# Kernel tuning notes

Hardware: AMD Instinct MI355X
Metric: run time of the kernel (lower is better)

The kernel has to match this reference:

```python
import jax, jax.numpy as jnp
import numpy as np

B, N = 4, 500
C_DIM = 256            # content_dim == feat_channels
G = 4                  # n_groups
P_IN, P_OUT = 32, 128
EFF = C_DIM // G       # 64 = eff_in_dim = eff_out_dim
TOTAL = EFF * EFF + P_IN * P_OUT   # 8192 params per group per query
STRIDES = (8, 16, 32, 64)
LVL_SHAPES = ((100, 160), (50, 80), (25, 40), (13, 20))
TAU = 2.0
LVL_MAP = 3.0          # log2(STRIDES[0]): z -> fpn level index
EPS = 1e-5


def setup_inputs() -> dict:
    key = jax.random.key(0)
    ks = jax.random.split(key, 16)
    feats = [jax.random.normal(ks[i], (B, C_DIM, h, w), jnp.float32)
             for i, (h, w) in enumerate(LVL_SHAPES)]
    query_feat = jax.random.normal(ks[4], (B, N, C_DIM), jnp.float32)
    xy = jax.random.uniform(ks[5], (B, N, 2), jnp.float32, 50.0, 1000.0)
    z = jax.random.uniform(ks[6], (B, N, 1), jnp.float32, 3.0, 6.0)
    r = jax.random.uniform(ks[7], (B, N, 1), jnp.float32, -1.0, 1.0)
    query_xyzr = jnp.concatenate([xy, z, r], -1)
    w_off = jax.random.normal(ks[8], (C_DIM, P_IN * G * 3), jnp.float32) * 0.01
    b_off = jax.random.normal(ks[9], (P_IN * G * 3,), jnp.float32) * 0.1
    w_pg = jax.random.normal(ks[10], (C_DIM, G * TOTAL), jnp.float32) * 0.02
    b_pg = jax.random.normal(ks[11], (G * TOTAL,), jnp.float32) * 0.02
    w_out = jax.random.normal(ks[12], (G * P_OUT * EFF, C_DIM), jnp.float32) * 0.005
    b_out = jnp.zeros((C_DIM,), jnp.float32)
    ln_g = jnp.ones((C_DIM,), jnp.float32)
    ln_b = jnp.zeros((C_DIM,), jnp.float32)
    return dict(feat0=feats[0], feat1=feats[1], feat2=feats[2], feat3=feats[3],
                query_feat=query_feat, query_xyzr=query_xyzr,
                w_off=w_off, b_off=b_off, w_pg=w_pg, b_pg=b_pg,
                w_out=w_out, b_out=b_out, ln_g=ln_g, ln_b=ln_b)


def _ln2d(x):
    # F.layer_norm over last TWO dims, no affine
    mu = x.mean((-2, -1), keepdims=True)
    var = jnp.mean((x - mu) ** 2, (-2, -1), keepdims=True)
    return (x - mu) * jax.lax.rsqrt(var + EPS)


def _bilinear(feat, px, py):
    # torch grid_sample(bilinear, zeros padding, align_corners=False)
    # feat: [BG, H, W, Cg]; px, py: [BG, Q] pixel coords
    BGn, H, W, Cg = feat.shape
    fflat = feat.reshape(BGn, H * W, Cg)
    bidx = jnp.arange(BGn)[:, None]
    x0 = jnp.floor(px)
    y0 = jnp.floor(py)
    wx, wy = px - x0, py - y0
    x0i, y0i = x0.astype(jnp.int32), y0.astype(jnp.int32)

    def corner(xi, yi, w):
        valid = (xi >= 0) & (xi < W) & (yi >= 0) & (yi < H)
        idx = jnp.clip(yi, 0, H - 1) * W + jnp.clip(xi, 0, W - 1)
        return fflat[bidx, idx] * (w * valid)[..., None]

    return (corner(x0i, y0i, (1 - wx) * (1 - wy)) + corner(x0i + 1, y0i, wx * (1 - wy))
            + corner(x0i, y0i + 1, (1 - wx) * wy) + corner(x0i + 1, y0i + 1, wx * wy))


def _forward(feat0, feat1, feat2, feat3, query_feat, query_xyzr,
             w_off, b_off, w_pg, b_pg, w_out, b_out, ln_g, ln_b):
    feats = (feat0, feat1, feat2, feat3)
    # --- make_sample_points ---
    off = (query_feat @ w_off + b_off).reshape(B, N, G * P_IN, 3)
    cc = query_xyzr[..., :2]
    z = query_xyzr[..., 2:3]
    r = query_xyzr[..., 3:4]
    roi_wh = (2.0 ** z) * jnp.concatenate([2.0 ** (-0.5 * r), 2.0 ** (0.5 * r)], -1)  # [B,N,2]
    sample_xy = cc[:, :, None, :] + off[..., :2] * roi_wh[:, :, None, :]   # [B,N,G*P,2]
    sample_lvl = z[:, :, None, 0:1] + off[..., 2:3]                        # [B,N,G*P,1]

    # --- sampling_3d: softmax level weights ---
    lvl = sample_lvl[..., 0] - LVL_MAP                                     # [B,N,G*P]
    grid = jnp.arange(len(STRIDES), dtype=lvl.dtype)
    lw = jax.nn.softmax(-((lvl[..., None] - grid) ** 2) / TAU, axis=-1)    # [B,N,G*P,L]

    # regroup to per-group layout [B*G, N*P, ...]
    sx = sample_xy.reshape(B, N, G, P_IN, 2).transpose(0, 2, 1, 3, 4).reshape(B * G, N * P_IN, 2)
    lw_g = lw.reshape(B, N, G, P_IN, -1).transpose(0, 2, 1, 3, 4).reshape(B * G, N * P_IN, -1)

    sampled = jnp.zeros((B * G, N * P_IN, EFF), jnp.float32)
    for li, (feat, stride) in enumerate(zip(feats, STRIDES)):
        H, W = feat.shape[2], feat.shape[3]
        fg = feat.reshape(B * G, EFF, H, W).transpose(0, 2, 3, 1)  # [BG,H,W,EFF]
        nx = sx[..., 0] / (W * stride) * 2.0 - 1.0
        ny = sx[..., 1] / (H * stride) * 2.0 - 1.0
        px = (nx + 1.0) * 0.5 * W - 0.5
        py = (ny + 1.0) * 0.5 * H - 0.5
        sampled = sampled + _bilinear(fg, px, py) * lw_g[..., li][..., None]
    # [B,N,G,P,EFF]
    x = sampled.reshape(B, G, N, P_IN, EFF).transpose(0, 2, 1, 3, 4)

    # --- AdaptiveMixing ---
    params = (query_feat @ w_pg + b_pg).reshape(B * N, G, TOTAL)
    M = params[..., :EFF * EFF].reshape(B * N, G, EFF, EFF)
    S = params[..., EFF * EFF:].reshape(B * N, G, P_OUT, P_IN)
    out = x.reshape(B * N, G, P_IN, EFF)
    out = jax.nn.relu(_ln2d(jnp.einsum('bgpc,bgcd->bgpd', out, M)))  # channel mix
    out = jax.nn.relu(_ln2d(jnp.einsum('bgop,bgpd->bgod', S, out)))  # spatial mix
    out = out.reshape(B, N, G * P_OUT * EFF) @ w_out + b_out
    q = query_feat + out

    # --- final LayerNorm(content_dim) with affine ---
    mu = q.mean(-1, keepdims=True)
    var = jnp.mean((q - mu) ** 2, -1, keepdims=True)
    return (q - mu) * jax.lax.rsqrt(var + EPS) * ln_g + ln_b


def reference(feat0, feat1, feat2, feat3, query_feat, query_xyzr,
              w_off, b_off, w_pg, b_pg, w_out, b_out, ln_g, ln_b):
    return _forward(feat0, feat1, feat2, feat3, query_feat, query_xyzr,
                    w_off, b_off, w_pg, b_pg, w_out, b_out, ln_g, ln_b)
```

## Files before the change

kernel.cpp:

```cpp
#include <hip/hip_runtime.h>
#include <hip/hip_bf16.h>
#include <cstdint>
#include <cstddef>

#define DI __device__ __forceinline__

#define NN 500
#define NQ 2000
#define GTOT 32768
#define LN_EPS 1e-5f

typedef __attribute__((ext_vector_type(8))) short short8v;
typedef __attribute__((ext_vector_type(4))) float f32x4;
typedef __attribute__((ext_vector_type(2))) float f32x2;
typedef const __attribute__((address_space(1))) void* gp1_t;
typedef __attribute__((address_space(3))) void* lp3_t;

DI unsigned short f2bf(float f){
  unsigned u = __float_as_uint(f);
  return (unsigned short)((u + 0x7fffu + ((u>>16)&1u)) >> 16);
}
DI float bf2f(unsigned short s){ return __uint_as_float(((unsigned)s)<<16); }

DI ushort4 cvt4(float4 a){
  ushort4 r; r.x=f2bf(a.x); r.y=f2bf(a.y); r.z=f2bf(a.z); r.w=f2bf(a.w); return r;
}

DI void bred256(float& s, float& s2, float* red, int tid){
  #pragma unroll
  for(int off=32; off; off>>=1){
    s  += __shfl_xor(s,  off, 64);
    s2 += __shfl_xor(s2, off, 64);
  }
  int w = tid>>6;
  if((tid&63)==0){ red[w*2]=s; red[w*2+1]=s2; }
  __syncthreads();
  s  = red[0]+red[2]+red[4]+red[6];
  s2 = red[1]+red[3]+red[5]+red[7];
  __syncthreads();
}

__global__ __launch_bounds__(384) void k_off(const float* __restrict__ qf,
    const float* __restrict__ xyzr, const float* __restrict__ w_off,
    const float* __restrict__ b_off, float2* __restrict__ xyb, float4* __restrict__ lwb){
  __shared__ float qs[8][256];
  __shared__ float os[8][384];
  int q0 = blockIdx.x*8, tid = threadIdx.x;
  for(int idx=tid; idx<2048; idx+=384){
    int qq = idx>>8, k = idx&255;
    qs[qq][k] = qf[(size_t)(q0+qq)*256 + k];
  }
  __syncthreads();
  {
    int j = tid;
    float acc[8];
    #pragma unroll
    for(int i=0;i<8;i++) acc[i]=0.f;
    for(int k=0;k<256;k++){
      float w = w_off[(size_t)k*384 + j];
      #pragma unroll
      for(int qq=0;qq<8;qq++) acc[qq] += qs[qq][k]*w;
    }
    float bb = b_off[j];
    #pragma unroll
    for(int qq=0;qq<8;qq++) os[qq][j] = acc[qq] + bb;
  }
  __syncthreads();
  for(int idx=tid; idx<1024; idx+=384){
    int qq = idx>>7, gp = idx&127;
    int q = q0+qq;
    float4 xr = *(const float4*)&xyzr[(size_t)q*4];
    float rw = exp2f(xr.z - 0.5f*xr.w);
    float rh = exp2f(xr.z + 0.5f*xr.w);
    float sx = xr.x + os[qq][gp*3+0]*rw;
    float sy = xr.y + os[qq][gp*3+1]*rh;
    float lvl = xr.z + os[qq][gp*3+2] - 3.0f;
    float d0=lvl, d1=lvl-1.f, d2=lvl-2.f, d3=lvl-3.f;
    float e0=-0.5f*d0*d0, e1=-0.5f*d1*d1, e2=-0.5f*d2*d2, e3=-0.5f*d3*d3;
    float m = fmaxf(fmaxf(e0,e1),fmaxf(e2,e3));
    float x0=expf(e0-m), x1=expf(e1-m), x2=expf(e2-m), x3=expf(e3-m);
    float inv = 1.f/(x0+x1+x2+x3);
    xyb[(size_t)q*128+gp] = make_float2(sx,sy);
    lwb[(size_t)q*128+gp] = make_float4(x0*inv, x1*inv, x2*inv, x3*inv);
  }
}

__global__ __launch_bounds__(256) void k_prep2(
    const float* __restrict__ f0, const float* __restrict__ f1,
    const float* __restrict__ f2, const float* __restrict__ f3,
    const float* __restrict__ qf, const float* __restrict__ w_pg,
    const float* __restrict__ w_out, unsigned short* __restrict__ featT,
    unsigned short* __restrict__ qfb, unsigned short* __restrict__ wpgT,
    unsigned short* __restrict__ woutT){
  __shared__ unsigned short tile[64*68];
  int bid = blockIdx.x, tid = threadIdx.x;

  if(bid < 4096){
    const float* src; unsigned short* dst; int R, C, lb;
    if(bid < 2048){ src=w_pg;  dst=wpgT;  R=256;  C=GTOT; lb=bid; }
    else          { src=w_out; dst=woutT; R=GTOT; C=256;  lb=bid-2048; }
    int ctiles = C >> 6;
    int rt = lb / ctiles, ct = lb % ctiles;
    int r0 = rt<<6, c0 = ct<<6;
    #pragma unroll
    for(int i=0;i<4;i++){
      int idx = tid + i*256;
      int r = idx >> 4, c4 = (idx & 15)*4;
      float4 v = *(const float4*)(src + (size_t)(r0+r)*C + c0 + c4);
      *(ushort4*)(tile + r*68 + c4) = cvt4(v);
    }
    __syncthreads();
    #pragma unroll
    for(int i=0;i<4;i++){
      int idx = tid + i*256;
      int cc = idx >> 4, r4 = (idx & 15)*4;
      ushort4 v;
      v.x = tile[(r4+0)*68 + cc];
      v.y = tile[(r4+1)*68 + cc];
      v.z = tile[(r4+2)*68 + cc];
      v.w = tile[(r4+3)*68 + cc];
      *(ushort4*)(dst + (size_t)(c0+cc)*R + r0 + r4) = v;
    }
  } else if(bid < 9440){
    const float* src; unsigned short* dst; int HW, nb, lb;
    int fb = bid - 4096;
    if(fb < 4000){ src=f0; dst=featT;            HW=16000; nb=250; lb=fb; }
    else if(fb < 5008){ src=f1; dst=featT+16384000; HW=4000; nb=63; lb=fb-4000; }
    else if(fb < 5264){ src=f2; dst=featT+20480000; HW=1000; nb=16; lb=fb-5008; }
    else { src=f3; dst=featT+21504000; HW=260; nb=5; lb=fb-5264; }
    int bg = lb / nb, hb = lb % nb;
    int b = bg >> 2, g = bg & 3;
    const float* s = src + ((size_t)(b*256 + g*64))*HW + hb*64;
    unsigned short* d = dst + (size_t)bg*HW*64 + (size_t)hb*64*64;
    int rem = HW - hb*64;
    #pragma unroll
    for(int i=0;i<4;i++){
      int idx = tid + i*256;
      int c = idx >> 4, h4 = (idx & 15)*4;
      if(h4 < rem){
        float4 v = *(const float4*)(s + (size_t)c*HW + h4);
        *(ushort4*)(tile + c*68 + h4) = cvt4(v);
      }
    }
    __syncthreads();
    #pragma unroll
    for(int i=0;i<4;i++){
      int idx = tid + i*256;
      int hw = idx >> 4, c4 = (idx & 15)*4;
      if(hw < rem){
        ushort4 v;
        v.x = tile[(c4+0)*68 + hw];
        v.y = tile[(c4+1)*68 + hw];
        v.z = tile[(c4+2)*68 + hw];
        v.w = tile[(c4+3)*68 + hw];
        *(ushort4*)(d + (size_t)hw*64 + c4) = v;
      }
    }
  } else {
    int idx = (bid-9440)*256 + tid;
    size_t base = (size_t)idx*8;
    int row = idx >> 5;
    ushort4 lo, hi;
    if(row < NQ){
      float4 a = *(const float4*)(qf + base);
      float4 b = *(const float4*)(qf + base + 4);
      lo = cvt4(a); hi = cvt4(b);
    } else {
      lo.x=lo.y=lo.z=lo.w=0; hi.x=hi.y=hi.z=hi.w=0;
    }
    *(ushort4*)(qfb + base) = lo;
    *(ushort4*)(qfb + base + 4) = hi;
  }
}

DI f32x4 mfma16(short8v a, short8v b, f32x4 c){
  return __builtin_amdgcn_mfma_f32_16x16x32_bf16(a, b, c, 0, 0, 0);
}

DI int swz32(int c, int r){ return c ^ (r&3) ^ ((r>>2)&3); }

DI void stageG32(const unsigned short* __restrict__ g, size_t row0, size_t ldk,
                 size_t k0, unsigned short* lds, int tid){
  int wv = tid>>6;
  #pragma unroll
  for(int i=0;i<2;i++){
    int e = i*256 + tid;
    int r = e>>2, c = e&3;
    int cs = swz32(c, r);
    const unsigned short* gp = g + (row0 + (size_t)r)*ldk + k0 + (size_t)cs*8;
    unsigned short* lp = lds + (size_t)(i*256 + wv*64)*8;
    __builtin_amdgcn_global_load_lds((gp1_t)(const void*)gp, (lp3_t)(void*)lp, 16, 0, 0);
  }
}

DI short8v frag32(const unsigned short* lds, int row, int q4){
  return *(const short8v*)(lds + (size_t)row*32 + (size_t)swz32(q4, row)*8);
}

DI void mma32(const unsigned short* lsA, const unsigned short* lsB,
              int wm, int wn, int lane, f32x4 acc[4][4]){
  int r15 = lane&15, q4 = lane>>4;
  short8v a[4], b[4];
  #pragma unroll
  for(int i=0;i<4;i++){
    a[i] = frag32(lsA, wm*64 + i*16 + r15, q4);
    b[i] = frag32(lsB, wn*64 + i*16 + r15, q4);
  }
  #pragma unroll
  for(int mi=0;mi<4;mi++)
    #pragma unroll
    for(int ni=0;ni<4;ni++)
      acc[mi][ni] = mfma16(a[mi], b[ni], acc[mi][ni]);
}

DI int xcd_remap(int bid, int nwg){
  return ((bid & 7) * (nwg >> 3)) + (bid >> 3);
}

__global__ __launch_bounds__(256, 4) void k_pgemm_mfma(const unsigned short* __restrict__ qfb,
    const unsigned short* __restrict__ wpgT, const float* __restrict__ b_pg,
    unsigned short* __restrict__ par, int qbase, int qlim, int mtiles){
  __shared__ unsigned short pool[16384];
  int bid = xcd_remap(blockIdx.x, gridDim.x);
  int mt = bid % mtiles, nt = bid / mtiles;
  size_t m0 = (size_t)mt*128, n0 = (size_t)nt*128;
  int tid = threadIdx.x, lane = tid&63, wv = tid>>6;
  int wm = wv>>1, wn = wv&1;
  int r15 = lane&15, q4 = lane>>4;
  f32x4 acc[4][4] = {};
  stageG32(qfb,  qbase+m0, 256, 0, pool, tid);
  stageG32(wpgT, n0,       256, 0, pool + 8192, tid);
  __syncthreads();
  #pragma unroll
  for(int t=0; t<8; t++){
    int co = (t&1)*4096;
    if(t<7){
      int no = ((t&1)^1)*4096;
      stageG32(qfb,  qbase+m0, 256, (size_t)(t+1)*32, pool + no, tid);
      stageG32(wpgT, n0,       256, (size_t)(t+1)*32, pool + 8192 + no, tid);
    }
    mma32(pool + co, pool + 8192 + co, wm, wn, lane, acc);
    __syncthreads();
  }
  unsigned short* es = pool;
  #pragma unroll
  for(int h=0; h<2; ++h){
    if(h) __syncthreads();
    if(wn == h){
      #pragma unroll
      for(int ni=0; ni<4; ni++){
        float bias = b_pg[(int)n0 + wn*64 + ni*16 + r15];
        #pragma unroll
        for(int mi=0; mi<4; mi++)
          #pragma unroll
          for(int j=0; j<4; j++){
            int row = wm*64 + mi*16 + q4*4 + j;
            es[row*72 + ni*16 + r15] = f2bf(acc[mi][ni][j] + bias);
          }
      }
    }
    __syncthreads();
    #pragma unroll
    for(int i=0;i<4;i++){
      int e = i*256 + tid;
      int row = e>>3, c8 = (e&7)*8;
      int rl = (int)m0 + row;
      if(qbase + rl < qlim){
        uint4 v = *(const uint4*)(es + row*72 + c8);
        *(uint4*)&par[(size_t)rl*GTOT + n0 + h*64 + c8] = v;
      }
    }
  }
}

__global__ __launch_bounds__(256, 4) void k_fgemm_mfma(const unsigned short* __restrict__ Ag,
    const unsigned short* __restrict__ woutT, float* __restrict__ part,
    int qbase, int qlim, int mtiles, int kspl){
  __shared__ unsigned short pool[16384];
  int bid = xcd_remap(blockIdx.x, gridDim.x);
  int nt = bid & 1;
  int r2 = bid >> 1;
  int mt = r2 % mtiles, ks = r2 / mtiles;
  size_t m0 = (size_t)mt*128, n0 = (size_t)nt*128;
  int tid = threadIdx.x, lane = tid&63, wv = tid>>6;
  int wm = wv>>1, wn = wv&1;
  f32x4 acc[4][4] = {};
  int klen = GTOT / kspl;
  size_t kbase = (size_t)ks*klen;
  int NT = klen >> 5;
  stageG32(Ag,    m0, GTOT, kbase, pool, tid);
  stageG32(woutT, n0, GTOT, kbase, pool + 8192, tid);
  __syncthreads();
  for(int t=0; t<NT; t++){
    int co = (t&1)*4096;
    if(t+1<NT){
      int no = ((t&1)^1)*4096;
      stageG32(Ag,    m0, GTOT, kbase + (size_t)(t+1)*32, pool + no, tid);
      stageG32(woutT, n0, GTOT, kbase + (size_t)(t+1)*32, pool + 8192 + no, tid);
    }
    mma32(pool + co, pool + 8192 + co, wm, wn, lane, acc);
    __syncthreads();
  }
  float* pp = part + (size_t)ks*NQ*256;
  int r15 = lane&15, q4 = lane>>4;
  #pragma unroll
  for(int mi=0; mi<4; mi++){
    #pragma unroll
    for(int j=0; j<4; j++){
      int rl = (int)m0 + wm*64 + mi*16 + q4*4 + j;
      int q = qbase + rl;
      if(q < qlim){
        #pragma unroll
        for(int ni=0; ni<4; ni++){
          int col = (int)n0 + wn*64 + ni*16 + r15;
          pp[(size_t)q*256 + col] = acc[mi][ni][j];
        }
      }
    }
  }
}

__global__ __launch_bounds__(256) void k_mix(const unsigned short* __restrict__ featT,
    const float2* __restrict__ xyb, const float4* __restrict__ lwb,
    const unsigned short* __restrict__ par, unsigned short* __restrict__ out2,
    int qbase){
  __shared__ __align__(16) char pool[31744];
  __shared__ float red[8];
  float* offW = (float*)pool;
  unsigned short* xs  = (unsigned short*)(pool + 4096);
  unsigned short* Ms  = (unsigned short*)(pool + 8704);
  unsigned short* o1t = (unsigned short*)(pool + 17408);
  unsigned short* Ss  = (unsigned short*)(pool + 22528);
  unsigned short* o2s = (unsigned short*)pool;

  int lq = blockIdx.x >> 2, g = blockIdx.x & 3;
  int q = qbase + lq;
  int b = q / NN;
  int bg = b*4 + g;
  int tid = threadIdx.x;
  int lane = tid & 63, wv = tid >> 6;

  const int HH[4] = {100,50,25,13};
  const int WW[4] = {160,80,40,20};
  const float IS[4] = {0.125f, 0.0625f, 0.03125f, 0.015625f};
  const int LO[4] = {0, 16384000, 20480000, 21504000};

  const unsigned short* pb = par + (size_t)lq*GTOT + (size_t)g*8192;
  uint4 mraw0 = *(const uint4*)(pb + tid*8);
  uint4 mraw1 = *(const uint4*)(pb + 2048 + tid*8);
  uint4 sraw0 = *(const uint4*)(pb + 4096 + tid*8);
  uint4 sraw1 = *(const uint4*)(pb + 6144 + tid*8);

  if(tid < 128){
    int p = tid >> 2, l = tid & 3;
    int pi = q*128 + g*32 + p;
    float2 xy = xyb[pi];
    float lw4 = ((const float*)lwb)[(size_t)pi*4 + l];
    int H = HH[l], W = WW[l];
    float px = xy.x*IS[l] - 0.5f;
    float py = xy.y*IS[l] - 0.5f;
    float xf = floorf(px), yf = floorf(py);
    float wx = px - xf, wy = py - yf;
    int x0 = (int)xf, y0 = (int)yf;
    int x1 = x0 + 1, y1 = y0 + 1;
    bool vx0 = (x0>=0)&&(x0<W), vx1 = (x1>=0)&&(x1<W);
    bool vy0 = (y0>=0)&&(y0<H), vy1 = (y1>=0)&&(y1<H);
    int x0c = min(max(x0,0),W-1), x1c = min(max(x1,0),W-1);
    int y0c = min(max(y0,0),H-1), y1c = min(max(y1,0),H-1);
    int baseB = (LO[l] + bg*H*W*64) * 2;
    float* e = offW + tid*8;
    e[0] = __int_as_float(baseB + (y0c*W + x0c)*128);
    e[1] = __int_as_float(baseB + (y0c*W + x1c)*128);
    e[2] = __int_as_float(baseB + (y1c*W + x0c)*128);
    e[3] = __int_as_float(baseB + (y1c*W + x1c)*128);
    e[4] = (1.f-wx)*(1.f-wy)*lw4*(float)(vx0&&vy0);
    e[5] = wx*(1.f-wy)*lw4*(float)(vx1&&vy0);
    e[6] = (1.f-wx)*wy*lw4*(float)(vx0&&vy1);
    e[7] = wx*wy*lw4*(float)(vx1&&vy1);
  }

  {
    int idx0 = tid*8;
    int c0 = idx0>>6, d0 = idx0&63;
    *(uint2*)(Ms + c0*68 + d0)     = make_uint2(mraw0.x, mraw0.y);
    *(uint2*)(Ms + c0*68 + d0 + 4) = make_uint2(mraw0.z, mraw0.w);
    int idx1 = 2048 + tid*8;
    int c1 = idx1>>6, d1 = idx1&63;
    *(uint2*)(Ms + c1*68 + d1)     = make_uint2(mraw1.x, mraw1.y);
    *(uint2*)(Ms + c1*68 + d1 + 4) = make_uint2(mraw1.z, mraw1.w);
    int o0 = idx0>>5, p0 = idx0&31;
    *(uint2*)(Ss + o0*36 + p0)     = make_uint2(sraw0.x, sraw0.y);
    *(uint2*)(Ss + o0*36 + p0 + 4) = make_uint2(sraw0.z, sraw0.w);
    int o1_ = idx1>>5, p1 = idx1&31;
    *(uint2*)(Ss + o1_*36 + p1)     = make_uint2(sraw1.x, sraw1.y);
    *(uint2*)(Ss + o1_*36 + p1 + 4) = make_uint2(sraw1.z, sraw1.w);
  }
  __syncthreads();

  {
    int half = lane >> 5, cp = lane & 31;
    const char* fbB = (const char*)featT + cp*4;
    #pragma unroll
    for(int i=0;i<4;i++){
      int p = wv*8 + i*2 + half;
      const float* e = offW + p*32;
      f32x2 acc2 = {0.f, 0.f};
      #pragma unroll
      for(int l=0;l<4;l++){
        int4  ea = *(const int4*)(e + l*8);
        float4 eb = *(const float4*)(e + l*8 + 4);
        unsigned u00 = *(const unsigned*)(fbB + ea.x);
        unsigned u01 = *(const unsigned*)(fbB + ea.y);
        unsigned u10 = *(const unsigned*)(fbB + ea.z);
        unsigned u11 = *(const unsigned*)(fbB + ea.w);
        f32x2 v00 = {__uint_as_float(u00<<16), __uint_as_float(u00&0xffff0000u)};
        f32x2 v01 = {__uint_as_float(u01<<16), __uint_as_float(u01&0xffff0000u)};
        f32x2 v10 = {__uint_as_float(u10<<16), __uint_as_float(u10&0xffff0000u)};
        f32x2 v11 = {__uint_as_float(u11<<16), __uint_as_float(u11&0xffff0000u)};
        acc2 += v00 * eb.x;
        acc2 += v01 * eb.y;
        acc2 += v10 * eb.z;
        acc2 += v11 * eb.w;
      }
      unsigned lo = f2bf(acc2.x), hi = f2bf(acc2.y);
      *(unsigned*)(xs + p*72 + cp*2) = lo | (hi<<16);
    }
  }
  __syncthreads();

  int r = lane & 15, q4 = lane >> 4;

  {
    short8v af00 = *(const short8v*)(xs + r*72 + q4*8);
    short8v af01 = *(const short8v*)(xs + r*72 + 32 + q4*8);
    short8v af10 = *(const short8v*)(xs + (16+r)*72 + q4*8);
    short8v af11 = *(const short8v*)(xs + (16+r)*72 + 32 + q4*8);
    short8v bm0, bm1;
    #pragma unroll
    for(int j=0;j<8;j++){
      bm0[j] = (short)Ms[(8*q4+j)*68 + wv*16 + r];
      bm1[j] = (short)Ms[(32+8*q4+j)*68 + wv*16 + r];
    }
    f32x4 a0 = {}, a1 = {};
    a0 = mfma16(af00, bm0, a0); a0 = mfma16(af01, bm1, a0);
    a1 = mfma16(af10, bm0, a1); a1 = mfma16(af11, bm1, a1);

    float s = 0.f, s2 = 0.f;
    #pragma unroll
    for(int v=0;v<4;v++){ s += a0[v]+a1[v]; s2 += a0[v]*a0[v] + a1[v]*a1[v]; }
    bred256(s, s2, red, tid);
    float mean = s*(1.f/2048.f);
    float var = s2*(1.f/2048.f) - mean*mean;
    float rs = rsqrtf(var + LN_EPS);
    ushort4 st0, st1;
    {
      float f0;
      f0 = (a0[0]-mean)*rs; st0.x = f2bf(f0>0.f?f0:0.f);
      f0 = (a0[1]-mean)*rs; st0.y = f2bf(f0>0.f?f0:0.f);
      f0 = (a0[2]-mean)*rs; st0.z = f2bf(f0>0.f?f0:0.f);
      f0 = (a0[3]-mean)*rs; st0.w = f2bf(f0>0.f?f0:0.f);
      f0 = (a1[0]-mean)*rs; st1.x = f2bf(f0>0.f?f0:0.f);
      f0 = (a1[1]-mean)*rs; st1.y = f2bf(f0>0.f?f0:0.f);
      f0 = (a1[2]-mean)*rs; st1.z = f2bf(f0>0.f?f0:0.f);
      f0 = (a1[3]-mean)*rs; st1.w = f2bf(f0>0.f?f0:0.f);
    }
    *(ushort4*)(o1t + (wv*16+r)*40 + 4*q4)      = st0;
    *(ushort4*)(o1t + (wv*16+r)*40 + 16 + 4*q4) = st1;
  }
  __syncthreads();

  {
    short8v sa0, sa1;
    {
      int row0 = (wv*2+0)*16 + r, row1 = (wv*2+1)*16 + r;
      uint2 a = *(const uint2*)(Ss + row0*36 + q4*8);
      uint2 bq = *(const uint2*)(Ss + row0*36 + q4*8 + 4);
      uint4 t0; t0.x=a.x; t0.y=a.y; t0.z=bq.x; t0.w=bq.y;
      sa0 = *(short8v*)&t0;
      a  = *(const uint2*)(Ss + row1*36 + q4*8);
      bq = *(const uint2*)(Ss + row1*36 + q4*8 + 4);
      uint4 t1; t1.x=a.x; t1.y=a.y; t1.z=bq.x; t1.w=bq.y;
      sa1 = *(short8v*)&t1;
    }
    short8v ov0 = *(const short8v*)(o1t + (r)*40 + q4*8);
    short8v ov1 = *(const short8v*)(o1t + (16+r)*40 + q4*8);
    short8v ov2 = *(const short8v*)(o1t + (32+r)*40 + q4*8);
    short8v ov3 = *(const short8v*)(o1t + (48+r)*40 + q4*8);
    f32x4 c2[2][4] = {};
    c2[0][0] = mfma16(sa0, ov0, c2[0][0]); c2[0][1] = mfma16(sa0, ov1, c2[0][1]);
    c2[0][2] = mfma16(sa0, ov2, c2[0][2]); c2[0][3] = mfma16(sa0, ov3, c2[0][3]);
    c2[1][0] = mfma16(sa1, ov0, c2[1][0]); c2[1][1] = mfma16(sa1, ov1, c2[1][1]);
    c2[1][2] = mfma16(sa1, ov2, c2[1][2]); c2[1][3] = mfma16(sa1, ov3, c2[1][3]);

    float s = 0.f, s2 = 0.f;
    #pragma unroll
    for(int m=0;m<2;m++)
      #pragma unroll
      for(int ni=0;ni<4;ni++)
        #pragma unroll
        for(int v=0;v<4;v++){ float x = c2[m][ni][v]; s += x; s2 += x*x; }
    bred256(s, s2, red, tid);
    float mean = s*(1.f/8192.f);
    float var = s2*(1.f/8192.f) - mean*mean;
    float rs = rsqrtf(var + LN_EPS);
    #pragma unroll
    for(int m=0;m<2;m++)
      #pragma unroll
      for(int ni=0;ni<4;ni++)
        #pragma unroll
        for(int v=0;v<4;v++){
          float x = (c2[m][ni][v]-mean)*rs; x = x>0.f ? x : 0.f;
          int o = (wv*2+m)*16 + 4*q4 + v;
          int d = ni*16 + r;
          o2s[o*72 + d] = f2bf(x);
        }
  }
  __syncthreads();

  unsigned short* og = out2 + (size_t)lq*GTOT + (size_t)g*8192;
  #pragma unroll
  for(int i=0;i<4;i++){
    int e = i*256 + tid;
    int row = e>>3, c8 = (e&7)*8;
    uint4 v = *(const uint4*)(o2s + row*72 + c8);
    *(uint4*)(og + row*64 + c8) = v;
  }
}

__global__ __launch_bounds__(256) void k_ln(const float* __restrict__ part,
    const float* __restrict__ qf, const float* __restrict__ b_out,
    const float* __restrict__ ln_g, const float* __restrict__ ln_b,
    float* __restrict__ out, int kspl){
  __shared__ float red[8];
  int q = blockIdx.x, j = threadIdx.x;
  float s = qf[(size_t)q*256 + j] + b_out[j];
  for(int ks=0; ks<kspl; ks++) s += part[((size_t)ks*NQ + q)*256 + j];
  float a = s, a2 = s*s;
  bred256(a, a2, red, j);
  float mean = a*(1.f/256.f);
  float var = a2*(1.f/256.f) - mean*mean;
  float rs = rsqrtf(var + LN_EPS);
  out[(size_t)q*256 + j] = (s-mean)*rs*ln_g[j] + ln_b[j];
}

extern "C" void kernel_launch(void* const* d_in, const int* in_sizes, int n_in,
                              void* d_out, int out_size, void* d_ws, size_t ws_size,
                              hipStream_t stream) {
  const float* feat0 = (const float*)d_in[0];
  const float* feat1 = (const float*)d_in[1];
  const float* feat2 = (const float*)d_in[2];
  const float* feat3 = (const float*)d_in[3];
  const float* qf    = (const float*)d_in[4];
  const float* xyzr  = (const float*)d_in[5];
  const float* w_off = (const float*)d_in[6];
  const float* b_off = (const float*)d_in[7];
  const float* w_pg  = (const float*)d_in[8];
  const float* b_pg  = (const float*)d_in[9];
  const float* w_out = (const float*)d_in[10];
  const float* b_out = (const float*)d_in[11];
  const float* ln_g  = (const float*)d_in[12];
  const float* ln_b  = (const float*)d_in[13];

  int KSP=0, NC=0, qcount=0, qpad=0;
  size_t oFEAT=0,oXY=0,oLW=0,oPART=0,oQFB=0,oWPGT=0,oWOUT=0,oPAR=0;
  {
    const int a_ksp[2] = {32, 16};
    for(int ci=0; ci<2 && NC==0; ci++){
      size_t o = 0;
      auto al = [&](size_t bytes){ size_t r = o; o = (o + bytes + 255) & ~255ull; return r; };
      size_t tFEAT = al(43540480ull);
      size_t tXY   = al((size_t)NQ*128*8);
      size_t tLW   = al((size_t)NQ*128*16);
      size_t tQFB  = al((size_t)2048*256*2);
      size_t tWPGT = al((size_t)GTOT*256*2);
      size_t partBytes = (size_t)a_ksp[ci]*NQ*256*4;
      if(partBytes > o) o = (partBytes + 255) & ~255ull;
      size_t tWOUT = al((size_t)256*GTOT*2);
      size_t tPAR  = al((size_t)2048*GTOT*2);
      if(o <= ws_size){
        KSP=a_ksp[ci]; NC=1; qcount=NQ; qpad=2048;
        oFEAT=tFEAT; oXY=tXY; oLW=tLW; oPART=0; oQFB=tQFB; oWPGT=tWPGT; oWOUT=tWOUT; oPAR=tPAR;
      }
    }
    const int c_nc[3] = {2,4,8};
    for(int ci=0; ci<3 && NC==0; ci++){
      size_t o = 0;
      auto al = [&](size_t bytes){ size_t r = o; o = (o + bytes + 255) & ~255ull; return r; };
      size_t tFEAT = al(43540480ull);
      size_t tXY   = al((size_t)NQ*128*8);
      size_t tLW   = al((size_t)NQ*128*16);
      size_t tPART = al((size_t)16*NQ*256*4);
      size_t tQFB  = al((size_t)2048*256*2);
      size_t tWPGT = al((size_t)GTOT*256*2);
      size_t tWOUT = al((size_t)256*GTOT*2);
      int qc = NQ / c_nc[ci];
      int qp = (qc + 127) & ~127;
      size_t tPAR = al((size_t)qp*GTOT*2);
      if(o <= ws_size){
        KSP=16; NC=c_nc[ci]; qcount=qc; qpad=qp;
        oFEAT=tFEAT; oXY=tXY; oLW=tLW; oPART=tPART; oQFB=tQFB; oWPGT=tWPGT; oWOUT=tWOUT; oPAR=tPAR;
      }
    }
  }
  if(NC == 0) return;

  char* ws = (char*)d_ws;
  unsigned short* featT = (unsigned short*)(ws + oFEAT);
  float2* xyb = (float2*)(ws + oXY);
  float4* lwb = (float4*)(ws + oLW);
  float* part = (float*)(ws + oPART);
  unsigned short* qfb  = (unsigned short*)(ws + oQFB);
  unsigned short* wpgT = (unsigned short*)(ws + oWPGT);
  unsigned short* woutT= (unsigned short*)(ws + oWOUT);
  unsigned short* par  = (unsigned short*)(ws + oPAR);
  unsigned short* o2   = par;

  k_off<<<250, 384, 0, stream>>>(qf, xyzr, w_off, b_off, xyb, lwb);
  k_prep2<<<9696, 256, 0, stream>>>(feat0, feat1, feat2, feat3, qf, w_pg, w_out,
                                    featT, qfb, wpgT, woutT);

  int mtiles = qpad / 128;
  for (int c = 0; c < NC; ++c) {
    int qbase = c * qcount;
    int qlim  = qbase + qcount;
    k_pgemm_mfma<<<mtiles*256, 256, 0, stream>>>(qfb, wpgT, b_pg, par, qbase, qlim, mtiles);
    k_mix<<<qcount*4, 256, 0, stream>>>(featT, xyb, lwb, par, o2, qbase);
    k_fgemm_mfma<<<mtiles*2*KSP, 256, 0, stream>>>(o2, woutT, part, qbase, qlim, mtiles, KSP);
  }
  k_ln<<<NQ, 256, 0, stream>>>(part, qf, b_out, ln_g, ln_b, (float*)d_out, KSP);
}
```

Before: 297.0 us.

## Raise GEMM launch-bound occupancy and widen bilinear gather to 4 channels per lane

Raises the minimum waves-per-SIMD hint from 4 to 5 on the parameter-generation and output GEMM kernels, pushing the compiler to use fewer registers so more workgroups can be resident. Separately, the bilinear sampling loop now has each lane gather 8-byte chunks (4 bf16 channels) instead of 4-byte chunks (2 channels). Each wave therefore handles 4 sample points per iteration over 2 iterations instead of 2 points over 4. The tighter register cap risks spills in the MFMA kernels, and wider gathers may change the LDS or cache access pattern.

```diff
diff --git a/kernel.cpp b/kernel.cpp
--- a/kernel.cpp
+++ b/kernel.cpp
@@ -217,7 +217,7 @@
   return ((bid & 7) * (nwg >> 3)) + (bid >> 3);
 }
 
-__global__ __launch_bounds__(256, 4) void k_pgemm_mfma(const unsigned short* __restrict__ qfb,
+__global__ __launch_bounds__(256, 5) void k_pgemm_mfma(const unsigned short* __restrict__ qfb,
     const unsigned short* __restrict__ wpgT, const float* __restrict__ b_pg,
     unsigned short* __restrict__ par, int qbase, int qlim, int mtiles){
   __shared__ unsigned short pool[16384];
@@ -273,7 +273,7 @@
   }
 }
 
-__global__ __launch_bounds__(256, 4) void k_fgemm_mfma(const unsigned short* __restrict__ Ag,
+__global__ __launch_bounds__(256, 5) void k_fgemm_mfma(const unsigned short* __restrict__ Ag,
     const unsigned short* __restrict__ woutT, float* __restrict__ part,
     int qbase, int qlim, int mtiles, int kspl){
   __shared__ unsigned short pool[16384];
@@ -398,32 +398,39 @@
   __syncthreads();
 
   {
-    int half = lane >> 5, cp = lane & 31;
-    const char* fbB = (const char*)featT + cp*4;
-    #pragma unroll
-    for(int i=0;i<4;i++){
-      int p = wv*8 + i*2 + half;
+    int pg4 = lane >> 4;
+    int cg  = lane & 15;
+    const char* fbB = (const char*)featT + cg*8;
+    #pragma unroll
+    for(int i=0;i<2;i++){
+      int p = wv*8 + i*4 + pg4;
       const float* e = offW + p*32;
-      f32x2 acc2 = {0.f, 0.f};
+      f32x4 acc4 = {0.f, 0.f, 0.f, 0.f};
       #pragma unroll
       for(int l=0;l<4;l++){
         int4  ea = *(const int4*)(e + l*8);
         float4 eb = *(const float4*)(e + l*8 + 4);
-        unsigned u00 = *(const unsigned*)(fbB + ea.x);
-        unsigned u01 = *(const unsigned*)(fbB + ea.y);
-        unsigned u10 = *(const unsigned*)(fbB + ea.z);
-        unsigned u11 = *(const unsigned*)(fbB + ea.w);
-        f32x2 v00 = {__uint_as_float(u00<<16), __uint_as_float(u00&0xffff0000u)};
-        f32x2 v01 = {__uint_as_float(u01<<16), __uint_as_float(u01&0xffff0000u)};
-        f32x2 v10 = {__uint_as_float(u10<<16), __uint_as_float(u10&0xffff0000u)};
-        f32x2 v11 = {__uint_as_float(u11<<16), __uint_as_float(u11&0xffff0000u)};
-        acc2 += v00 * eb.x;
-        acc2 += v01 * eb.y;
-        acc2 += v10 * eb.z;
-        acc2 += v11 * eb.w;
-      }
-      unsigned lo = f2bf(acc2.x), hi = f2bf(acc2.y);
-      *(unsigned*)(xs + p*72 + cp*2) = lo | (hi<<16);
+        uint2 u00 = *(const uint2*)(fbB + ea.x);
+        uint2 u01 = *(const uint2*)(fbB + ea.y);
+        uint2 u10 = *(const uint2*)(fbB + ea.z);
+        uint2 u11 = *(const uint2*)(fbB + ea.w);
+        f32x4 v;
+        v[0]=__uint_as_float(u00.x<<16); v[1]=__uint_as_float(u00.x&0xffff0000u);
+        v[2]=__uint_as_float(u00.y<<16); v[3]=__uint_as_float(u00.y&0xffff0000u);
+        acc4 += v * eb.x;
+        v[0]=__uint_as_float(u01.x<<16); v[1]=__uint_as_float(u01.x&0xffff0000u);
+        v[2]=__uint_as_float(u01.y<<16); v[3]=__uint_as_float(u01.y&0xffff0000u);
+        acc4 += v * eb.y;
+        v[0]=__uint_as_float(u10.x<<16); v[1]=__uint_as_float(u10.x&0xffff0000u);
+        v[2]=__uint_as_float(u10.y<<16); v[3]=__uint_as_float(u10.y&0xffff0000u);
+        acc4 += v * eb.z;
+        v[0]=__uint_as_float(u11.x<<16); v[1]=__uint_as_float(u11.x&0xffff0000u);
+        v[2]=__uint_as_float(u11.y<<16); v[3]=__uint_as_float(u11.y&0xffff0000u);
+        acc4 += v * eb.w;
+      }
+      unsigned w0 = (unsigned)f2bf(acc4[0]) | ((unsigned)f2bf(acc4[1])<<16);
+      unsigned w1 = (unsigned)f2bf(acc4[2]) | ((unsigned)f2bf(acc4[3])<<16);
+      *(uint2*)(xs + p*72 + cg*4) = make_uint2(w0, w1);
     }
   }
   __syncthreads();
```

Result: slower. 333.3 us (+12.2%).
